# Performance work log

Measured on AMD Instinct MI355X. Metric: run time of the kernel, lower is better.

The kernel has to match this reference:

```python
import jax, jax.numpy as jnp
import numpy as np

B, S, D = 2, 4096, 2048
EPS = 1e-6


def rms_norm(x):
    return x * jax.lax.rsqrt(jnp.mean(x * x, axis=-1, keepdims=True) + EPS)


def setup_inputs() -> dict:
    key = jax.random.key(0)
    ks = jax.random.split(key, 6)
    w_scale = 1.0 / np.sqrt(D)
    return {
        "v": jax.random.normal(ks[0], (B, S, D), dtype=jnp.float32),
        "out": jax.random.normal(ks[1], (B, S, D), dtype=jnp.float32),
        "c": jax.random.normal(ks[2], (B, S, D), dtype=jnp.float32),
        "prev_fetched": jax.random.normal(ks[3], (B, S, D), dtype=jnp.float32),
        "W_alpha": jax.random.normal(ks[4], (D, D), dtype=jnp.float32) * w_scale,
        "b_alpha": jnp.linspace(0.0, 8.0, D, dtype=jnp.float32),  # step_idx=1 bias init
        "W_beta": jax.random.normal(ks[5], (D, D), dtype=jnp.float32) * w_scale,
        "b_beta": jnp.zeros((D,), dtype=jnp.float32),
        "g_out": jnp.ones((D,), dtype=jnp.float32),   # out-gate default init
        "g_v": jnp.zeros((D,), dtype=jnp.float32),    # v-gate init.zeros
    }


def reference(v, out, c, prev_fetched, W_alpha, b_alpha, W_beta, b_beta, g_out, g_v):
    # step_idx = 1 -> gate_input includes prev_fetched norm
    gate_input = rms_norm(c) + rms_norm(prev_fetched)  # [B,S,D]
    alphas = jax.nn.sigmoid(gate_input @ W_alpha + b_alpha)  # [B,S,D]
    betas = jax.nn.silu(gate_input @ W_beta + b_beta)        # [B,S,D]
    write_scale = jnp.sqrt(jnp.maximum(1.0 - alphas * alphas, 1e-6))
    x = v * betas * write_scale

    # linear recurrence h_t = alpha_t * h_{t-1} + x_t via associative scan over seq axis
    def combine(a, b):
        x_i, a_i = a
        x_j, a_j = b
        return (a_j * x_i + x_j, a_j * a_i)

    fetched, _ = jax.lax.associative_scan(combine, (x, alphas), axis=1)

    out_new = out + fetched * g_out
    v_new = v + fetched * g_v
    return (v_new, out_new, c, fetched)
```

## Files before the change

### kernel.cpp

```cpp
#include <hip/hip_runtime.h>

#define B_ 2
#define S_ 4096
#define D_ 2048
#define M_ (B_ * S_)
#define EPSV 1e-6f
#define CT 64
#define NCHUNK (S_ / CT)
#define LOG_NCHUNK 6

static_assert(NCHUNK == (1 << LOG_NCHUNK), "chunk math");

#define BM 128
#define BN 128
#define BK 32

typedef __bf16 bf16x8 __attribute__((ext_vector_type(8)));
typedef __bf16 bf16x4 __attribute__((ext_vector_type(4)));
typedef float  f32x4  __attribute__((ext_vector_type(4)));

__device__ __bf16 g_gate[(size_t)M_ * D_];
__device__ __bf16 g_WtA[(size_t)D_ * D_];
__device__ __bf16 g_WtB[(size_t)D_ * D_];
__device__ float  g_alpha[(size_t)M_ * D_];
__device__ float  g_x[(size_t)M_ * D_];
__device__ float  g_pa[B_ * NCHUNK * D_];
__device__ float  g_ph[B_ * NCHUNK * D_];

__global__ __launch_bounds__(256) void k_pre(const float* __restrict__ c,
                                             const float* __restrict__ pf,
                                             float* __restrict__ c_out) {
  const int row = blockIdx.x;
  const int t = threadIdx.x;
  const size_t rb = (size_t)row * D_;
  const float4* c4 = (const float4*)(c + rb);
  const float4* p4 = (const float4*)(pf + rb);
  float4 cv0 = c4[t], cv1 = c4[t + 256];
  float4 pv0 = p4[t], pv1 = p4[t + 256];
  float ssc = cv0.x*cv0.x + cv0.y*cv0.y + cv0.z*cv0.z + cv0.w*cv0.w
            + cv1.x*cv1.x + cv1.y*cv1.y + cv1.z*cv1.z + cv1.w*cv1.w;
  float ssp = pv0.x*pv0.x + pv0.y*pv0.y + pv0.z*pv0.z + pv0.w*pv0.w
            + pv1.x*pv1.x + pv1.y*pv1.y + pv1.z*pv1.z + pv1.w*pv1.w;
  #pragma unroll
  for (int off = 32; off; off >>= 1) {
    ssc += __shfl_down(ssc, off);
    ssp += __shfl_down(ssp, off);
  }
  __shared__ float red[8];
  const int wave = t >> 6, lane = t & 63;
  if (lane == 0) { red[wave] = ssc; red[wave + 4] = ssp; }
  __syncthreads();
  const float sc = red[0] + red[1] + red[2] + red[3];
  const float sp = red[4] + red[5] + red[6] + red[7];
  const float rc = rsqrtf(sc * (1.0f / D_) + EPSV);
  const float rp = rsqrtf(sp * (1.0f / D_) + EPSV);
  bf16x4 o0 = { (__bf16)(cv0.x*rc + pv0.x*rp), (__bf16)(cv0.y*rc + pv0.y*rp),
                (__bf16)(cv0.z*rc + pv0.z*rp), (__bf16)(cv0.w*rc + pv0.w*rp) };
  bf16x4 o1 = { (__bf16)(cv1.x*rc + pv1.x*rp), (__bf16)(cv1.y*rc + pv1.y*rp),
                (__bf16)(cv1.z*rc + pv1.z*rp), (__bf16)(cv1.w*rc + pv1.w*rp) };
  *(bf16x4*)(g_gate + rb + 4 * t) = o0;
  *(bf16x4*)(g_gate + rb + 1024 + 4 * t) = o1;
  f32x4* co = (f32x4*)(c_out + rb);
  __builtin_nontemporal_store(*(const f32x4*)&cv0, co + t);
  __builtin_nontemporal_store(*(const f32x4*)&cv1, co + t + 256);
}

__global__ __launch_bounds__(256) void k_wt(const float* __restrict__ Wa,
                                            const float* __restrict__ Wb) {
  __shared__ float tile[32][33];
  const float* W = blockIdx.z ? Wb : Wa;
  __bf16* outp = blockIdx.z ? g_WtB : g_WtA;
  const int n0 = blockIdx.x * 32, k0 = blockIdx.y * 32;
  for (int i = threadIdx.y; i < 32; i += 8)
    tile[i][threadIdx.x] = W[(size_t)(k0 + i) * D_ + n0 + threadIdx.x];
  __syncthreads();
  for (int i = threadIdx.y; i < 32; i += 8)
    outp[(size_t)(n0 + i) * D_ + k0 + threadIdx.x] = (__bf16)tile[threadIdx.x][i];
}

__device__ __forceinline__ void gld16(const void* g, void* l) {
  __builtin_amdgcn_global_load_lds((const __attribute__((address_space(1))) void*)g,
                                   (__attribute__((address_space(3))) void*)l, 16, 0, 0);
}
__device__ __forceinline__ f32x4 mfma16(bf16x8 a, bf16x8 b, f32x4 c) {
  return __builtin_amdgcn_mfma_f32_16x16x32_bf16(a, b, c, 0, 0, 0);
}

__global__ __launch_bounds__(256) void k_gemm(const float* __restrict__ v,
                                              const float* __restrict__ bia,
                                              const float* __restrict__ bib) {
  __shared__ __bf16 sA[BM * BK];
  __shared__ __bf16 sBa[BN * BK];
  __shared__ __bf16 sBb[BN * BK];
  const int tid = threadIdx.x;
  const int wave = tid >> 6, lane = tid & 63;
  const int bm = blockIdx.x, bn = blockIdx.y;
  const int wm = (wave >> 1) * 64, wn = (wave & 1) * 64;
  const int qd = lane >> 4, ln = lane & 15;

  const __bf16* gA  = g_gate + (size_t)(bm * BM) * D_;
  const __bf16* gBa = g_WtA + (size_t)(bn * BN) * D_;
  const __bf16* gBb = g_WtB + (size_t)(bn * BN) * D_;
  const int sr = tid >> 2;
  const int scc = (tid & 3) * 8;
  char* sAc = (char*)sA; char* sBac = (char*)sBa; char* sBbc = (char*)sBb;
  const int wb = wave * 1024;

  f32x4 acc_a[4][4], acc_b[4][4];
  #pragma unroll
  for (int i = 0; i < 4; i++)
    #pragma unroll
    for (int j = 0; j < 4; j++) {
      acc_a[i][j] = (f32x4){0.f, 0.f, 0.f, 0.f};
      acc_b[i][j] = (f32x4){0.f, 0.f, 0.f, 0.f};
    }

  for (int k0 = 0; k0 < D_; k0 += BK) {
    __syncthreads();
    gld16(gA  + (size_t)sr * D_ + k0 + scc,        sAc + wb);
    gld16(gA  + (size_t)(sr + 64) * D_ + k0 + scc, sAc + 4096 + wb);
    gld16(gBa + (size_t)sr * D_ + k0 + scc,        sBac + wb);
    gld16(gBa + (size_t)(sr + 64) * D_ + k0 + scc, sBac + 4096 + wb);
    gld16(gBb + (size_t)sr * D_ + k0 + scc,        sBbc + wb);
    gld16(gBb + (size_t)(sr + 64) * D_ + k0 + scc, sBbc + 4096 + wb);
    __syncthreads();
    bf16x8 af[4], bA[4], bB[4];
    #pragma unroll
    for (int i = 0; i < 4; i++)
      af[i] = *(const bf16x8*)(sA + (wm + i * 16 + ln) * BK + qd * 8);
    #pragma unroll
    for (int j = 0; j < 4; j++) {
      bA[j] = *(const bf16x8*)(sBa + (wn + j * 16 + ln) * BK + qd * 8);
      bB[j] = *(const bf16x8*)(sBb + (wn + j * 16 + ln) * BK + qd * 8);
    }
    #pragma unroll
    for (int i = 0; i < 4; i++)
      #pragma unroll
      for (int j = 0; j < 4; j++) {
        acc_a[i][j] = mfma16(af[i], bA[j], acc_a[i][j]);
        acc_b[i][j] = mfma16(af[i], bB[j], acc_b[i][j]);
      }
  }

  #pragma unroll
  for (int j = 0; j < 4; j++) {
    const int gn = bn * BN + wn + j * 16 + ln;
    const float baj = bia[gn], bbj = bib[gn];
    #pragma unroll
    for (int i = 0; i < 4; i++) {
      #pragma unroll
      for (int r = 0; r < 4; r++) {
        const int gm = bm * BM + wm + i * 16 + qd * 4 + r;
        const size_t idx = (size_t)gm * D_ + gn;
        const float za = acc_a[i][j][r] + baj;
        const float alpha = 1.0f / (1.0f + __expf(-za));
        const float zb = acc_b[i][j][r] + bbj;
        const float beta = zb / (1.0f + __expf(-zb));
        const float wsq = sqrtf(fmaxf(1.0f - alpha * alpha, 1e-6f));
        g_alpha[idx] = alpha;
        g_x[idx] = v[idx] * beta * wsq;
      }
    }
  }
}

__global__ __launch_bounds__(256) void k_scan1() {
  const int bid = blockIdx.x;
  const int dblk = bid & 7;
  const int cg = bid >> 3;
  const int chunk = cg & (NCHUNK - 1);
  const int b = cg >> LOG_NCHUNK;
  const int d = dblk * 256 + threadIdx.x;
  const size_t base = ((size_t)b * S_ + (size_t)chunk * CT) * D_ + d;
  float h = 0.f, p = 1.f;
  #pragma unroll 4
  for (int t = 0; t < CT; ++t) {
    const float a = g_alpha[base + (size_t)t * D_];
    const float x = g_x[base + (size_t)t * D_];
    h = a * h + x;
    p *= a;
  }
  const int pi = (b * NCHUNK + chunk) * D_ + d;
  g_pa[pi] = p;
  g_ph[pi] = h;
}

__global__ __launch_bounds__(256) void k_scan2() {
  const int ch = blockIdx.x * 256 + threadIdx.x;
  const int b = ch >> 11, dd = ch & (D_ - 1);
  float carry = 0.f;
  #pragma unroll
  for (int chunk = 0; chunk < NCHUNK; ++chunk) {
    const int pi = (b * NCHUNK + chunk) * D_ + dd;
    const float p = g_pa[pi];
    const float h = g_ph[pi];
    g_ph[pi] = carry;
    carry = p * carry + h;
  }
}

__global__ __launch_bounds__(256) void k_scan3(const float* __restrict__ v,
                                               const float* __restrict__ outp,
                                               const float* __restrict__ go_,
                                               const float* __restrict__ gv_,
                                               float* __restrict__ v_new,
                                               float* __restrict__ out_new,
                                               float* __restrict__ fetched) {
  const int bid = blockIdx.x;
  const int dblk = bid & 7;
  const int cg = bid >> 3;
  const int chunk = cg & (NCHUNK - 1);
  const int b = cg >> LOG_NCHUNK;
  const int d = dblk * 256 + threadIdx.x;
  const int pi = (b * NCHUNK + chunk) * D_ + d;
  float h = g_ph[pi];
  const float go = go_[d], gv = gv_[d];
  const size_t base = ((size_t)b * S_ + (size_t)chunk * CT) * D_ + d;
  #pragma unroll 4
  for (int t = 0; t < CT; ++t) {
    const size_t idx = base + (size_t)t * D_;
    const float a = g_alpha[idx];
    const float x = g_x[idx];
    h = a * h + x;
    __builtin_nontemporal_store(h, fetched + idx);
    __builtin_nontemporal_store(outp[idx] + h * go, out_new + idx);
    __builtin_nontemporal_store(v[idx] + h * gv, v_new + idx);
  }
}

extern "C" void kernel_launch(void* const* d_in, const int* in_sizes, int n_in,
                              void* d_out, int out_size, void* d_ws, size_t ws_size,
                              hipStream_t stream) {
  const float* v   = (const float*)d_in[0];
  const float* out = (const float*)d_in[1];
  const float* c   = (const float*)d_in[2];
  const float* pf  = (const float*)d_in[3];
  const float* Wa  = (const float*)d_in[4];
  const float* ba  = (const float*)d_in[5];
  const float* Wb  = (const float*)d_in[6];
  const float* bb  = (const float*)d_in[7];
  const float* go  = (const float*)d_in[8];
  const float* gv  = (const float*)d_in[9];

  float* obase = (float*)d_out;
  const size_t BSD = (size_t)B_ * S_ * D_;
  float* v_new   = obase;
  float* out_new = obase + BSD;
  float* c_out   = obase + 2 * BSD;
  float* fetched = obase + 3 * BSD;

  hipLaunchKernelGGL(k_wt,   dim3(D_ / 32, D_ / 32, 2), dim3(32, 8), 0, stream, Wa, Wb);
  hipLaunchKernelGGL(k_pre,  dim3(M_), dim3(256), 0, stream, c, pf, c_out);
  hipLaunchKernelGGL(k_gemm, dim3(M_ / BM, D_ / BN), dim3(256), 0, stream, v, ba, bb);
  hipLaunchKernelGGL(k_scan1, dim3(B_ * NCHUNK * (D_ / 256)), dim3(256), 0, stream);
  hipLaunchKernelGGL(k_scan2, dim3((B_ * D_) / 256), dim3(256), 0, stream);
  hipLaunchKernelGGL(k_scan3, dim3(B_ * NCHUNK * (D_ / 256)), dim3(256), 0, stream,
                     v, out, go, gv, v_new, out_new, fetched);
}
```

Baseline: 936.8 us.

## Split dual-output GEMM into separate alpha and beta blocks, move write-scale to scans

The fused GEMM that computed both alpha and beta accumulators in one block is split so that each block computes only one of them, doubling the grid along N. This halves accumulator registers and LDS per block, which should raise occupancy, but the A tile is now loaded twice. Because alpha and beta are no longer in the same block, the write-scale sqrt is moved into both scan kernels, which recompute x from the stored alpha and v*beta.

```diff
diff --git a/kernel.cpp b/kernel.cpp
--- a/kernel.cpp
+++ b/kernel.cpp
@@ -14,6 +14,7 @@
 #define BM 128
 #define BN 128
 #define BK 32
+#define NB_ (D_ / BN)
 
 typedef __bf16 bf16x8 __attribute__((ext_vector_type(8)));
 typedef __bf16 bf16x4 __attribute__((ext_vector_type(4)));
@@ -23,7 +24,7 @@
 __device__ __bf16 g_WtA[(size_t)D_ * D_];
 __device__ __bf16 g_WtB[(size_t)D_ * D_];
 __device__ float  g_alpha[(size_t)M_ * D_];
-__device__ float  g_x[(size_t)M_ * D_];
+__device__ float  g_bv[(size_t)M_ * D_];
 __device__ float  g_pa[B_ * NCHUNK * D_];
 __device__ float  g_ph[B_ * NCHUNK * D_];
 
@@ -90,75 +91,81 @@
                                               const float* __restrict__ bia,
                                               const float* __restrict__ bib) {
   __shared__ __bf16 sA[BM * BK];
-  __shared__ __bf16 sBa[BN * BK];
-  __shared__ __bf16 sBb[BN * BK];
+  __shared__ __bf16 sB[BN * BK];
   const int tid = threadIdx.x;
   const int wave = tid >> 6, lane = tid & 63;
   const int bm = blockIdx.x, bn = blockIdx.y;
+  const int isBeta = bn >= NB_;
+  const int bnl = isBeta ? bn - NB_ : bn;
   const int wm = (wave >> 1) * 64, wn = (wave & 1) * 64;
   const int qd = lane >> 4, ln = lane & 15;
 
-  const __bf16* gA  = g_gate + (size_t)(bm * BM) * D_;
-  const __bf16* gBa = g_WtA + (size_t)(bn * BN) * D_;
-  const __bf16* gBb = g_WtB + (size_t)(bn * BN) * D_;
+  const __bf16* gA = g_gate + (size_t)(bm * BM) * D_;
+  const __bf16* gB = (isBeta ? g_WtB : g_WtA) + (size_t)(bnl * BN) * D_;
   const int sr = tid >> 2;
   const int scc = (tid & 3) * 8;
-  char* sAc = (char*)sA; char* sBac = (char*)sBa; char* sBbc = (char*)sBb;
+  char* sAc = (char*)sA; char* sBc = (char*)sB;
   const int wb = wave * 1024;
 
-  f32x4 acc_a[4][4], acc_b[4][4];
+  f32x4 acc[4][4];
   #pragma unroll
   for (int i = 0; i < 4; i++)
     #pragma unroll
-    for (int j = 0; j < 4; j++) {
-      acc_a[i][j] = (f32x4){0.f, 0.f, 0.f, 0.f};
-      acc_b[i][j] = (f32x4){0.f, 0.f, 0.f, 0.f};
-    }
+    for (int j = 0; j < 4; j++)
+      acc[i][j] = (f32x4){0.f, 0.f, 0.f, 0.f};
 
   for (int k0 = 0; k0 < D_; k0 += BK) {
     __syncthreads();
-    gld16(gA  + (size_t)sr * D_ + k0 + scc,        sAc + wb);
-    gld16(gA  + (size_t)(sr + 64) * D_ + k0 + scc, sAc + 4096 + wb);
-    gld16(gBa + (size_t)sr * D_ + k0 + scc,        sBac + wb);
-    gld16(gBa + (size_t)(sr + 64) * D_ + k0 + scc, sBac + 4096 + wb);
-    gld16(gBb + (size_t)sr * D_ + k0 + scc,        sBbc + wb);
-    gld16(gBb + (size_t)(sr + 64) * D_ + k0 + scc, sBbc + 4096 + wb);
+    gld16(gA + (size_t)sr * D_ + k0 + scc,        sAc + wb);
+    gld16(gA + (size_t)(sr + 64) * D_ + k0 + scc, sAc + 4096 + wb);
+    gld16(gB + (size_t)sr * D_ + k0 + scc,        sBc + wb);
+    gld16(gB + (size_t)(sr + 64) * D_ + k0 + scc, sBc + 4096 + wb);
     __syncthreads();
-    bf16x8 af[4], bA[4], bB[4];
+    bf16x8 af[4], bf[4];
     #pragma unroll
     for (int i = 0; i < 4; i++)
       af[i] = *(const bf16x8*)(sA + (wm + i * 16 + ln) * BK + qd * 8);
     #pragma unroll
-    for (int j = 0; j < 4; j++) {
-      bA[j] = *(const bf16x8*)(sBa + (wn + j * 16 + ln) * BK + qd * 8);
-      bB[j] = *(const bf16x8*)(sBb + (wn + j * 16 + ln) * BK + qd * 8);
-    }
+    for (int j = 0; j < 4; j++)
+      bf[j] = *(const bf16x8*)(sB + (wn + j * 16 + ln) * BK + qd * 8);
     #pragma unroll
     for (int i = 0; i < 4; i++)
       #pragma unroll
-      for (int j = 0; j < 4; j++) {
-        acc_a[i][j] = mfma16(af[i], bA[j], acc_a[i][j]);
-        acc_b[i][j] = mfma16(af[i], bB[j], acc_b[i][j]);
+      for (int j = 0; j < 4; j++)
+        acc[i][j] = mfma16(af[i], bf[j], acc[i][j]);
+  }
+
+  if (!isBeta) {
+    #pragma unroll
+    for (int j = 0; j < 4; j++) {
+      const int gn = bnl * BN + wn + j * 16 + ln;
+      const float baj = bia[gn];
+      #pragma unroll
+      for (int i = 0; i < 4; i++) {
+        #pragma unroll
+        for (int r = 0; r < 4; r++) {
+          const int gm = bm * BM + wm + i * 16 + qd * 4 + r;
+          const size_t idx = (size_t)gm * D_ + gn;
+          const float za = acc[i][j][r] + baj;
+          g_alpha[idx] = 1.0f / (1.0f + __expf(-za));
+        }
       }
-  }
-
-  #pragma unroll
-  for (int j = 0; j < 4; j++) {
-    const int gn = bn * BN + wn + j * 16 + ln;
-    const float baj = bia[gn], bbj = bib[gn];
-    #pragma unroll
-    for (int i = 0; i < 4; i++) {
+    }
+  } else {
+    #pragma unroll
+    for (int j = 0; j < 4; j++) {
+      const int gn = bnl * BN + wn + j * 16 + ln;
+      const float bbj = bib[gn];
       #pragma unroll
-      for (int r = 0; r < 4; r++) {
-        const int gm = bm * BM + wm + i * 16 + qd * 4 + r;
-        const size_t idx = (size_t)gm * D_ + gn;
-        const float za = acc_a[i][j][r] + baj;
-        const float alpha = 1.0f / (1.0f + __expf(-za));
-        const float zb = acc_b[i][j][r] + bbj;
-        const float beta = zb / (1.0f + __expf(-zb));
-        const float wsq = sqrtf(fmaxf(1.0f - alpha * alpha, 1e-6f));
-        g_alpha[idx] = alpha;
-        g_x[idx] = v[idx] * beta * wsq;
+      for (int i = 0; i < 4; i++) {
+        #pragma unroll
+        for (int r = 0; r < 4; r++) {
+          const int gm = bm * BM + wm + i * 16 + qd * 4 + r;
+          const size_t idx = (size_t)gm * D_ + gn;
+          const float zb = acc[i][j][r] + bbj;
+          const float beta = zb / (1.0f + __expf(-zb));
+          g_bv[idx] = v[idx] * beta;
+        }
       }
     }
   }
@@ -176,7 +183,8 @@
   #pragma unroll 4
   for (int t = 0; t < CT; ++t) {
     const float a = g_alpha[base + (size_t)t * D_];
-    const float x = g_x[base + (size_t)t * D_];
+    const float bv = g_bv[base + (size_t)t * D_];
+    const float x = bv * sqrtf(fmaxf(1.0f - a * a, 1e-6f));
     h = a * h + x;
     p *= a;
   }
@@ -220,7 +228,8 @@
   for (int t = 0; t < CT; ++t) {
     const size_t idx = base + (size_t)t * D_;
     const float a = g_alpha[idx];
-    const float x = g_x[idx];
+    const float bv = g_bv[idx];
+    const float x = bv * sqrtf(fmaxf(1.0f - a * a, 1e-6f));
     h = a * h + x;
     __builtin_nontemporal_store(h, fetched + idx);
     __builtin_nontemporal_store(outp[idx] + h * go, out_new + idx);
@@ -251,7 +260,7 @@
 
   hipLaunchKernelGGL(k_wt,   dim3(D_ / 32, D_ / 32, 2), dim3(32, 8), 0, stream, Wa, Wb);
   hipLaunchKernelGGL(k_pre,  dim3(M_), dim3(256), 0, stream, c, pf, c_out);
-  hipLaunchKernelGGL(k_gemm, dim3(M_ / BM, D_ / BN), dim3(256), 0, stream, v, ba, bb);
+  hipLaunchKernelGGL(k_gemm, dim3(M_ / BM, 2 * NB_), dim3(256), 0, stream, v, ba, bb);
   hipLaunchKernelGGL(k_scan1, dim3(B_ * NCHUNK * (D_ / 256)), dim3(256), 0, stream);
   hipLaunchKernelGGL(k_scan2, dim3((B_ * D_) / 256), dim3(256), 0, stream);
   hipLaunchKernelGGL(k_scan3, dim3(B_ * NCHUNK * (D_ / 256)), dim3(256), 0, stream,
```

New measurement: 819.2 us. -12.5%, faster.
